# Kernel optimization log

Measured on AMD Instinct MI355X. Metric: run time of the kernel, lower is better.

The kernel has to match this reference:

```python
import math
import jax, jax.numpy as jnp
import numpy as np

G_RATIO = 0.5
TB_FACTOR = 1e-3


def _expand(x):
    # x: [B,H,W]; 3x3 all-ones-except-center neighbor conv (same filter for every sample)
    k = jnp.ones((1, 1, 3, 3), x.dtype).at[0, 0, 1, 1].set(0.0)
    y = jax.lax.conv_general_dilated(x[:, None], k, (1, 1), 'SAME')
    return y[:, 0]


def _st_softmax_noexp(val):
    # straight-through normalized selection over flattened map
    B = val.shape[0]
    v = val.reshape(B, -1)
    y = v / v.sum(-1, keepdims=True)
    ind = jnp.argmax(y, -1)
    y_hard = jax.nn.one_hot(ind, y.shape[-1], dtype=y.dtype)
    y = y + jax.lax.stop_gradient(y_hard - y)
    return y.reshape(val.shape)


def _heuristic(gm):
    # gm: [B,H,W] one-hot goal maps -> Chebyshev + tb*Euclidean distance field
    B, H, W = gm.shape
    loc = jnp.stack(jnp.meshgrid(jnp.arange(H), jnp.arange(W), indexing='ij'), 0).astype(gm.dtype)  # [2,H,W]
    loc_e = loc.reshape(2, -1)[None]                      # [1,2,HW]
    goal_loc = jnp.einsum('kij,bij->bk', loc, gm)[:, :, None]  # [B,2,1]
    d = jnp.abs(loc_e - goal_loc)                         # [B,2,HW]
    h = d.sum(1) - d.min(1)
    euc = jnp.sqrt(((loc_e - goal_loc) ** 2).sum(1))
    return (h + TB_FACTOR * euc).reshape(B, H, W)


def _forward_core(cost_maps, start_maps, goal_maps, obstacles_maps):
    cm, sm, gm, om = cost_maps[:, 0], start_maps[:, 0], goal_maps[:, 0], obstacles_maps[:, 0]
    B, H, W = cm.shape
    h = _heuristic(gm) + cm
    goal_idx = jnp.argmax(gm.reshape(B, -1), -1)
    parents0 = jnp.broadcast_to(goal_idx[:, None].astype(cm.dtype), (B, H * W))
    inv_sqrt = 1.0 / math.sqrt(W)
    Tmax = W * W

    def step(carry, i):
        g, open_m, hist, parents, done, t = carry
        f = G_RATIO * g + (1.0 - G_RATIO) * h
        f_exp = jnp.exp(-f * inv_sqrt) * open_m
        snm = _st_softmax_noexp(f_exp)
        dist = (snm * gm).sum((1, 2), keepdims=True)
        unsolved = (dist < 1e-8).astype(cm.dtype)
        hist_n = jnp.clip(hist + snm, 0.0, 1.0)
        open_n = jnp.clip(open_m - unsolved * snm, 0.0, 1.0)
        nb = _expand(snm) * om
        g2 = _expand((g + cm) * snm)
        idx = ((1.0 - open_n) * (1.0 - hist_n) + open_n * (g > g2).astype(cm.dtype)) * nb
        idx = jax.lax.stop_gradient(idx)
        g_n = jax.lax.stop_gradient(g2 * idx + g * (1.0 - idx))
        open_n = jax.lax.stop_gradient(jnp.clip(open_n + idx, 0.0, 1.0))
        idx_f = idx.reshape(B, -1)
        new_par = jnp.argmax(snm.reshape(B, -1), -1)[:, None].astype(cm.dtype)
        par_n = new_par * idx_f + parents * (1.0 - idx_f)
        done_n = jnp.all(unsolved == 0)
        sel = lambda new, old: jnp.where(done, old, new)  # emulate the torch early break
        carry_n = (sel(g_n, g), sel(open_n, open_m), sel(hist_n, hist), sel(par_n, parents),
                   jnp.logical_or(done, done_n), jnp.where(done, t, i))
        return carry_n, None

    init = (jnp.zeros_like(sm), sm, jnp.zeros_like(sm), parents0,
            jnp.array(False), jnp.array(0, jnp.int32))
    (g, open_m, hist, parents, done, t), _ = jax.lax.scan(
        step, init, jnp.arange(Tmax, dtype=jnp.int32))
    return hist[:, None], parents, t


def _backtrack(goal_maps, parents, t):
    gm = goal_maps[:, 0]
    B, H, W = gm.shape
    par_i = parents.astype(jnp.int32)
    goal_f = gm.reshape(B, -1).astype(jnp.int32)
    loc = (par_i * goal_f).sum(-1)
    rng = jnp.arange(B)

    def bt(i, val):
        path, loc = val
        path = path.at[rng, loc].set(1)
        loc = jnp.take_along_axis(par_i, loc[:, None], -1)[:, 0]
        return (path, loc)

    path, _ = jax.lax.fori_loop(0, t, bt, (goal_f, loc))
    return path.reshape(B, 1, H, W)


def setup_inputs() -> dict:
    key = jax.random.key(0)
    k1, k2, k3, k4 = jax.random.split(key, 4)
    B, H, W = 16, 32, 32
    cost_maps = jax.random.uniform(k1, (B, 1, H, W), dtype=jnp.float32)
    sidx = jax.random.randint(k2, (B,), 0, H * W)
    gidx = jax.random.randint(k3, (B,), 0, H * W)
    gidx = jnp.where(gidx == sidx, (gidx + 1) % (H * W), gidx)
    start_maps = jax.nn.one_hot(sidx, H * W, dtype=jnp.float32).reshape(B, 1, H, W)
    goal_maps = jax.nn.one_hot(gidx, H * W, dtype=jnp.float32).reshape(B, 1, H, W)
    obstacles_maps = (jax.random.uniform(k4, (B, 1, H, W)) > 0.05).astype(jnp.float32)
    obstacles_maps = jnp.clip(obstacles_maps + start_maps + goal_maps, 0.0, 1.0)
    return {'cost_maps': cost_maps, 'start_maps': start_maps,
            'goal_maps': goal_maps, 'obstacles_maps': obstacles_maps}


def reference(cost_maps, start_maps, goal_maps, obstacles_maps):
    histories, parents, t = _forward_core(cost_maps, start_maps, goal_maps, obstacles_maps)
    path_maps = _backtrack(goal_maps, parents, t)
    return histories, path_maps
```

## Files before the change

kernel.cpp:

```cpp
#include <hip/hip_runtime.h>
#include <math.h>

#define HW 1024
#define NB 16
#define TMAXS 1024

typedef unsigned long long ull;

__device__ __forceinline__ double u2d(ull u) {
  return __longlong_as_double((long long)u);
}
__device__ __forceinline__ ull d2u(double d) {
  return (ull)__double_as_longlong(d);
}

__device__ __forceinline__ float keyhalf(float gh, float hh) {
#pragma clang fp contract(off)
  const float INV = 0.17677669529663687f;
  return expf(-(gh + hh) * INV);
}

__device__ __forceinline__ ull packkey(float keyf, int idx) {
  return ((ull)__float_as_uint(keyf) << 32) | (ull)(1023 - idx);
}

template <int CTRL>
__device__ __forceinline__ double dpp_fmax64(double x) {
  ull u = d2u(x);
  int lo = (int)(unsigned)u;
  int hi = (int)(unsigned)(u >> 32);
  int lo2 = __builtin_amdgcn_update_dpp(0, lo, CTRL, 0xF, 0xF, false);
  int hi2 = __builtin_amdgcn_update_dpp(0, hi, CTRL, 0xF, 0xF, false);
  double y = u2d(((ull)(unsigned)hi2 << 32) | (unsigned)lo2);
  return fmax(x, y);
}

extern "C" __global__ void __launch_bounds__(64) astar_fused(
    const float* __restrict__ cm_g, const float* __restrict__ sm_g,
    const float* __restrict__ gm_g, const float* __restrict__ om_g,
    float* __restrict__ out) {
#pragma clang fp contract(off)
  const int b = blockIdx.x;
  const int lane = threadIdx.x;

  __shared__ __align__(16) uint4 cellT[HW];
  __shared__ __align__(16) ull key2[HW];
  __shared__ __align__(16) unsigned par[HW];
  __shared__ __align__(16) ull level1[64];
  const float2* cell2 = (const float2*)cellT;
  unsigned* cellu = (unsigned*)cellT;

  const float* cm = cm_g + b * HW;
  const float* sm = sm_g + b * HW;
  const float* gm = gm_g + b * HW;
  const float* om = om_g + b * HW;

  float4 c4[4], o4[4];
  int gi = -1, si = -1;
#pragma unroll
  for (int q = 0; q < 4; ++q) {
    const int base = q * 256 + lane * 4;
    c4[q] = *(const float4*)(cm + base);
    o4[q] = *(const float4*)(om + base);
    const float4 s4 = *(const float4*)(sm + base);
    const float4 g4 = *(const float4*)(gm + base);
    const float sv[4] = {s4.x, s4.y, s4.z, s4.w};
    const float gv[4] = {g4.x, g4.y, g4.z, g4.w};
#pragma unroll
    for (int j = 0; j < 4; ++j) {
      if (gv[j] > 0.5f) gi = base + j;
      if (sv[j] > 0.5f) si = base + j;
    }
  }
#pragma unroll
  for (int m = 32; m >= 1; m >>= 1) {
    const int og = __shfl_xor(gi, m, 64);
    const int os = __shfl_xor(si, m, 64);
    gi = (og > gi) ? og : gi;
    si = (os > si) ? os : si;
  }
  const int goal = __builtin_amdgcn_readfirstlane(gi);
  const int start = __builtin_amdgcn_readfirstlane(si);

  level1[lane] = 0ull;
  const float grf = (float)(goal >> 5), gcf = (float)(goal & 31);
#pragma unroll
  for (int q = 0; q < 4; ++q) {
    const int base = q * 256 + lane * 4;
    const float cv[4] = {c4[q].x, c4[q].y, c4[q].z, c4[q].w};
    const float ov[4] = {o4[q].x, o4[q].y, o4[q].z, o4[q].w};
    ull pk[4];
#pragma unroll
    for (int j = 0; j < 4; ++j) {
      const int cell = base + j;
      const float rr = (float)(cell >> 5), cc = (float)(cell & 31);
      const float dr = fabsf(rr - grf), dc = fabsf(cc - gcf);
      const float h0 = (dr + dc) - fminf(dr, dc);
      const float euc = sqrtf(dr * dr + dc * dc);
      const float t1 = 0.001f * euc;
      const float hh = h0 + t1;
      const float hf = hh + cv[j];
      const float hw = 0.5f * hf;
      unsigned fv = (ov[j] > 0.5f) ? 1u : 0u;
      pk[j] = (ull)(1023 - cell);
      if (cell == start) {
        fv |= 2u;
        pk[j] = packkey(keyhalf(0.0f, hw), cell);
      }
      cellT[cell] = make_uint4(__float_as_uint(0.0f), __float_as_uint(cv[j]),
                               __float_as_uint(hw), fv);
      atomicMax(&level1[cell >> 4], pk[j]);
    }
    *(uint4*)&par[base] =
        make_uint4((unsigned)goal, (unsigned)goal, (unsigned)goal, (unsigned)goal);
    ulonglong2 k01, k23;
    k01.x = pk[0]; k01.y = pk[1];
    k23.x = pk[2]; k23.y = pk[3];
    *(ulonglong2*)&key2[base] = k01;
    *(ulonglong2*)&key2[base + 2] = k23;
  }
  __builtin_amdgcn_wave_barrier();
  ull stale = level1[lane];

  int dlt = 0;
  if (lane < 8) {
    const int k = (lane < 4) ? lane : lane + 1;
    dlt = (k / 3 - 1) * 32 + (k % 3 - 1);
  }

  int sel = start;
  bool reached = false;

#pragma unroll 1
  for (int step = 0; step < TMAXS; ++step) {
    if (sel == goal) { reached = true; break; }
    const int gp = sel >> 4;

    const int sr = sel >> 5, sc = sel & 31;
    unsigned vmask = 0xFFu;
    if (sr == 0) vmask &= ~0x07u;
    if (sr == 31) vmask &= ~0xE0u;
    if (sc == 0) vmask &= ~0x29u;
    if (sc == 31) vmask &= ~0x94u;

    const float2 sg = cell2[2 * sel];
    const int n = sel + dlt;
    const bool relaxer = (lane < 8) && ((vmask >> lane) & 1u);
    uint4 nv = make_uint4(0u, 0u, 0u, 0u);
    if (relaxer) nv = cellT[n];
    const bool gcl = (lane >= 16) && (lane < 32);
    const int gcell = gp * 16 + (lane - 16);
    ull gco = 0ull;
    if (gcl) gco = key2[gcell];

    double ma = (lane == gp) ? 0.0 : u2d(stale);
    ma = dpp_fmax64<0x111>(ma);
    ma = dpp_fmax64<0x112>(ma);
    ma = dpp_fmax64<0x114>(ma);
    ma = dpp_fmax64<0x118>(ma);
    ma = dpp_fmax64<0x142>(ma);
    ma = dpp_fmax64<0x143>(ma);

    const float g2full = sg.x + sg.y;
    const float g2h = 0.5f * g2full;
    const unsigned f = nv.w;
    bool updv = false;
    ull pk = 0ull;
    if (relaxer) {
      updv = (f & 1u) &&
             (((f & 6u) == 0u) ||
              (((f & 2u) != 0u) && (__uint_as_float(nv.x) > g2full)));
      if (updv) pk = packkey(keyhalf(g2h, __uint_as_float(nv.z)), n);
    }
    ull gcp = gco;
    if (gcl && gcell == sel) gcp = (ull)(1023 - sel);

    if (updv) {
      cellT[n] = make_uint4(__float_as_uint(g2full), nv.y, nv.z, f | 2u);
      par[n] = (unsigned)sel;
      key2[n] = pk;
    }
    if (lane == 8) {
      cellu[4 * sel + 3] = 5u;
      key2[sel] = (ull)(1023 - sel);
    }

    double ml = 0.0;
    if (gcl) ml = u2d(gcp);
    if (updv) ml = u2d(pk);
    ml = dpp_fmax64<0x111>(ml);
    ml = dpp_fmax64<0x112>(ml);
    ml = dpp_fmax64<0x114>(ml);
    ml = dpp_fmax64<0x118>(ml);

    if (lane == 31) level1[gp] = d2u(ml);
    if (updv) atomicMax(&level1[n >> 4], pk);
    const ull stale_n = level1[lane];

    const ull mlb = d2u(ml);
    const ull mab = d2u(ma);
    const int b_lo = __builtin_amdgcn_readlane((int)(unsigned)mlb, 15);
    const int b_hi = __builtin_amdgcn_readlane((int)(unsigned)(mlb >> 32), 15);
    const int c_lo = __builtin_amdgcn_readlane((int)(unsigned)mlb, 31);
    const int c_hi = __builtin_amdgcn_readlane((int)(unsigned)(mlb >> 32), 31);
    const int a_lo = __builtin_amdgcn_readlane((int)(unsigned)mab, 63);
    const int a_hi = __builtin_amdgcn_readlane((int)(unsigned)(mab >> 32), 63);
    const ull B2 = ((ull)(unsigned)b_hi << 32) | (unsigned)b_lo;
    const ull C2 = ((ull)(unsigned)c_hi << 32) | (unsigned)c_lo;
    const ull A2 = ((ull)(unsigned)a_hi << 32) | (unsigned)a_lo;
    ull M = (B2 > C2) ? B2 : C2;
    M = (M > A2) ? M : A2;
    sel = 1023 - (int)((unsigned)M & 1023u);
    stale = stale_n;
    __builtin_amdgcn_wave_barrier();
  }
  if (reached && lane == 0) cellu[4 * goal + 3] |= 4u;
  __builtin_amdgcn_wave_barrier();

  if (lane == 0) {
    const unsigned pv = par[goal];
    par[goal] = pv | 0x80000000u;
    unsigned loc = pv & 1023u;
#pragma unroll 1
    for (int i = 0; i < HW; ++i) {
      const unsigned w = par[loc];
      if (w & 0x80000000u) break;
      par[loc] = w | 0x80000000u;
      loc = w & 1023u;
    }
  }
  __builtin_amdgcn_wave_barrier();

#pragma unroll
  for (int q = 0; q < 4; ++q) {
    const int base = q * 256 + lane * 4;
    float4 hv, pv;
    hv.x = (cellu[4 * (base + 0) + 3] & 4u) ? 1.0f : 0.0f;
    hv.y = (cellu[4 * (base + 1) + 3] & 4u) ? 1.0f : 0.0f;
    hv.z = (cellu[4 * (base + 2) + 3] & 4u) ? 1.0f : 0.0f;
    hv.w = (cellu[4 * (base + 3) + 3] & 4u) ? 1.0f : 0.0f;
    pv.x = (par[base + 0] >> 31) ? 1.0f : 0.0f;
    pv.y = (par[base + 1] >> 31) ? 1.0f : 0.0f;
    pv.z = (par[base + 2] >> 31) ? 1.0f : 0.0f;
    pv.w = (par[base + 3] >> 31) ? 1.0f : 0.0f;
    *(float4*)(out + b * HW + base) = hv;
    *(float4*)(out + NB * HW + b * HW + base) = pv;
  }
}

extern "C" void kernel_launch(void* const* d_in, const int* in_sizes, int n_in,
                              void* d_out, int out_size, void* d_ws,
                              size_t ws_size, hipStream_t stream) {
  const float* cm = (const float*)d_in[0];
  const float* sm = (const float*)d_in[1];
  const float* gm = (const float*)d_in[2];
  const float* om = (const float*)d_in[3];
  float* out = (float*)d_out;
  hipLaunchKernelGGL(astar_fused, dim3(NB), dim3(64), 0, stream, cm, sm, gm,
                     om, out);
}
```

Baseline: 76.49 us.

## Speculatively prefetch neighbor data for likely next selected cells in A* loop

Each iteration now predicts two candidates for the next selected cell and loads their cost, neighbor and group-key data from LDS before the current iteration's argmax is resolved. The first candidate is the best among existing entries, the second is the newly relaxed neighbor with the smallest heuristic. If the actual selection matches a candidate, its prefetched values are reused, taking the dependent LDS loads off the serial critical path. The level-1 group update moves to atomicMax, and the max reduction over relaxed keys is split from the reduction over group keys. In exchange each step issues extra speculative LDS loads plus min/ballot/readlane work, and the prefetched data could be stale if writes in the same step touch those cells.

```diff
diff --git a/kernel.cpp b/kernel.cpp
--- a/kernel.cpp
+++ b/kernel.cpp
@@ -33,6 +33,31 @@
   int hi2 = __builtin_amdgcn_update_dpp(0, hi, CTRL, 0xF, 0xF, false);
   double y = u2d(((ull)(unsigned)hi2 << 32) | (unsigned)lo2);
   return fmax(x, y);
+}
+
+template <int CTRL>
+__device__ __forceinline__ unsigned dpp_minu32(unsigned x) {
+  int s = __builtin_amdgcn_update_dpp(0x7F800000, (int)x, CTRL, 0xF, 0xF,
+                                      false);
+  unsigned u = (unsigned)s;
+  return (x < u) ? x : u;
+}
+
+__device__ __forceinline__ ull rdl64(double d, int l) {
+  ull u = d2u(d);
+  int lo = __builtin_amdgcn_readlane((int)(unsigned)u, l);
+  int hi = __builtin_amdgcn_readlane((int)(unsigned)(u >> 32), l);
+  return ((ull)(unsigned)hi << 32) | (unsigned)lo;
+}
+
+__device__ __forceinline__ unsigned vmask_of(int cell) {
+  unsigned m = 0xFFu;
+  const int r = cell >> 5, c = cell & 31;
+  if (r == 0) m &= ~0x07u;
+  if (r == 31) m &= ~0xE0u;
+  if (c == 0) m &= ~0x29u;
+  if (c == 31) m &= ~0x94u;
+  return m;
 }
 
 extern "C" __global__ void __launch_bounds__(64) astar_fused(
@@ -131,27 +156,36 @@
   int sel = start;
   bool reached = false;
 
+  int spec1 = -1, spec2 = -1;
+  float2 sg1p = make_float2(0.f, 0.f), sg2p = make_float2(0.f, 0.f);
+  uint4 nv1p = make_uint4(0u, 0u, 0u, 0u), nv2p = make_uint4(0u, 0u, 0u, 0u);
+  ull gco1p = 0ull, gco2p = 0ull;
+
 #pragma unroll 1
   for (int step = 0; step < TMAXS; ++step) {
     if (sel == goal) { reached = true; break; }
     const int gp = sel >> 4;
-
-    const int sr = sel >> 5, sc = sel & 31;
-    unsigned vmask = 0xFFu;
-    if (sr == 0) vmask &= ~0x07u;
-    if (sr == 31) vmask &= ~0xE0u;
-    if (sc == 0) vmask &= ~0x29u;
-    if (sc == 31) vmask &= ~0x94u;
-
-    const float2 sg = cell2[2 * sel];
+    const unsigned vmask = vmask_of(sel);
     const int n = sel + dlt;
     const bool relaxer = (lane < 8) && ((vmask >> lane) & 1u);
-    uint4 nv = make_uint4(0u, 0u, 0u, 0u);
-    if (relaxer) nv = cellT[n];
     const bool gcl = (lane >= 16) && (lane < 32);
     const int gcell = gp * 16 + (lane - 16);
-    ull gco = 0ull;
-    if (gcl) gco = key2[gcell];
+
+    if (lane == 16) level1[gp] = 0ull;
+
+    const bool h1 = (sel == spec1), h2 = (sel == spec2);
+    float2 sg; uint4 nv; ull gco;
+    if (h1) {
+      sg = sg1p; nv = nv1p; gco = gco1p;
+    } else if (h2) {
+      sg = sg2p; nv = nv2p; gco = gco2p;
+    } else {
+      sg = cell2[2 * sel];
+      nv = make_uint4(0u, 0u, 0u, 0u);
+      if (relaxer) nv = cellT[n];
+      gco = 0ull;
+      if (gcl) gco = key2[gcell];
+    }
 
     double ma = (lane == gp) ? 0.0 : u2d(stale);
     ma = dpp_fmax64<0x111>(ma);
@@ -164,54 +198,80 @@
     const float g2full = sg.x + sg.y;
     const float g2h = 0.5f * g2full;
     const unsigned f = nv.w;
-    bool updv = false;
-    ull pk = 0ull;
-    if (relaxer) {
-      updv = (f & 1u) &&
-             (((f & 6u) == 0u) ||
-              (((f & 2u) != 0u) && (__uint_as_float(nv.x) > g2full)));
-      if (updv) pk = packkey(keyhalf(g2h, __uint_as_float(nv.z)), n);
-    }
-    ull gcp = gco;
-    if (gcl && gcell == sel) gcp = (ull)(1023 - sel);
-
+    const bool updv =
+        relaxer && (f & 1u) &&
+        (((f & 6u) == 0u) || (((f & 2u) != 0u) && (__uint_as_float(nv.x) > g2full)));
     if (updv) {
       cellT[n] = make_uint4(__float_as_uint(g2full), nv.y, nv.z, f | 2u);
       par[n] = (unsigned)sel;
-      key2[n] = pk;
     }
     if (lane == 8) {
       cellu[4 * sel + 3] = 5u;
       key2[sel] = (ull)(1023 - sel);
     }
 
-    double ml = 0.0;
-    if (gcl) ml = u2d(gcp);
-    if (updv) ml = u2d(pk);
-    ml = dpp_fmax64<0x111>(ml);
-    ml = dpp_fmax64<0x112>(ml);
-    ml = dpp_fmax64<0x114>(ml);
-    ml = dpp_fmax64<0x118>(ml);
-
-    if (lane == 31) level1[gp] = d2u(ml);
+    ull gcp = gco;
+    if (gcl && gcell == sel) gcp = (ull)(1023 - sel);
+    if (gcl) atomicMax(&level1[gp], gcp);
+
+    double mc = gcl ? u2d(gcp) : 0.0;
+    mc = dpp_fmax64<0x111>(mc);
+    mc = dpp_fmax64<0x112>(mc);
+    mc = dpp_fmax64<0x114>(mc);
+    mc = dpp_fmax64<0x118>(mc);
+
+    const unsigned hb = updv ? nv.z : 0x7F800000u;
+    unsigned mh = hb;
+    mh = dpp_minu32<0x111>(mh);
+    mh = dpp_minu32<0x112>(mh);
+    mh = dpp_minu32<0x114>(mh);
+    const unsigned MH = (unsigned)__builtin_amdgcn_readlane((int)mh, 7);
+    const bool valid2 = (MH != 0x7F800000u);
+    const ull bal = __ballot(updv && (hb == MH));
+    int l2 = (int)__ffsll(bal) - 1;
+    if (l2 < 0) l2 = 0;
+    const int s2 = __builtin_amdgcn_readlane(n, l2);
+
+    const unsigned vm2 = vmask_of(s2);
+    const bool rel2 = (lane < 8) && ((vm2 >> lane) & 1u);
+    sg2p = cell2[2 * s2];
+    nv2p = make_uint4(0u, 0u, 0u, 0u);
+    if (rel2) nv2p = cellT[s2 + dlt];
+
+    ull pk = 0ull;
+    if (updv) pk = packkey(keyhalf(g2h, __uint_as_float(nv.z)), n);
+    if (updv) key2[n] = pk;
     if (updv) atomicMax(&level1[n >> 4], pk);
     const ull stale_n = level1[lane];
 
-    const ull mlb = d2u(ml);
-    const ull mab = d2u(ma);
-    const int b_lo = __builtin_amdgcn_readlane((int)(unsigned)mlb, 15);
-    const int b_hi = __builtin_amdgcn_readlane((int)(unsigned)(mlb >> 32), 15);
-    const int c_lo = __builtin_amdgcn_readlane((int)(unsigned)mlb, 31);
-    const int c_hi = __builtin_amdgcn_readlane((int)(unsigned)(mlb >> 32), 31);
-    const int a_lo = __builtin_amdgcn_readlane((int)(unsigned)mab, 63);
-    const int a_hi = __builtin_amdgcn_readlane((int)(unsigned)(mab >> 32), 63);
-    const ull B2 = ((ull)(unsigned)b_hi << 32) | (unsigned)b_lo;
-    const ull C2 = ((ull)(unsigned)c_hi << 32) | (unsigned)c_lo;
-    const ull A2 = ((ull)(unsigned)a_hi << 32) | (unsigned)a_lo;
-    ull M = (B2 > C2) ? B2 : C2;
-    M = (M > A2) ? M : A2;
-    sel = 1023 - (int)((unsigned)M & 1023u);
+    gco2p = 0ull;
+    if (gcl) gco2p = key2[(s2 >> 4) * 16 + (lane - 16)];
+
+    double mb = updv ? u2d(pk) : 0.0;
+    mb = dpp_fmax64<0x111>(mb);
+    mb = dpp_fmax64<0x112>(mb);
+    mb = dpp_fmax64<0x114>(mb);
+
+    const ull GC = rdl64(mc, 31);
+    const ull MA = rdl64(ma, 63);
+    const ull PB = rdl64(mb, 7);
+    const ull MACv = (GC > MA) ? GC : MA;
+    const ull M = (PB > MACv) ? PB : MACv;
+    const int nsel = 1023 - (int)((unsigned)M & 1023u);
+    const int s1 = 1023 - (int)((unsigned)MACv & 1023u);
+
+    const unsigned vm1 = vmask_of(s1);
+    const bool rel1 = (lane < 8) && ((vm1 >> lane) & 1u);
+    sg1p = cell2[2 * s1];
+    nv1p = make_uint4(0u, 0u, 0u, 0u);
+    if (rel1) nv1p = cellT[s1 + dlt];
+    gco1p = 0ull;
+    if (gcl) gco1p = key2[(s1 >> 4) * 16 + (lane - 16)];
+
+    spec1 = s1;
+    spec2 = valid2 ? s2 : -1;
     stale = stale_n;
+    sel = nsel;
     __builtin_amdgcn_wave_barrier();
   }
   if (reached && lane == 0) cellu[4 * goal + 3] |= 4u;
```

Result: slower. 107.2 us (+40.1%).
